# Performance work log

Measured on AMD Instinct MI355X. Metric: run time of the kernel, lower is better.

The kernel has to match this reference:

```python
import jax, jax.numpy as jnp
import numpy as np

S, V, L = 64, 16, 5            # hn_dim=(64,16), num_layers=5
ED, RD, TD = 16, 16, 64        # edge_dim, rbf_dim, t_dim
N, EL, EG, B = 16384, 131072, 262144, 64
FIN = 2 * S + RD + ED          # per-edge message input width
H = S + 2 * V                  # message output: scalar msg + 2 vector gates
CUT_L, CUT_G = 3.0, 10.0


def _ln(x, g, b, eps=1e-5):
    m = x.mean(-1, keepdims=True)
    var = ((x - m) ** 2).mean(-1, keepdims=True)
    return (x - m) / jnp.sqrt(var + eps) * g + b


def _seg_mean(x, idx, n):
    s = jax.ops.segment_sum(x, idx, num_segments=n)
    c = jax.ops.segment_sum(jnp.ones((x.shape[0], 1), x.dtype), idx, num_segments=n)
    return s / jnp.maximum(c, 1.0)


def _edge_geom(ei, pos, cutoff):
    src, tgt = ei[0], ei[1]
    r = pos[tgt] - pos[src]                       # [E,3]
    d = jnp.sqrt(jnp.clip((r * r).sum(-1), 1e-6))
    rn = r / d[:, None]
    centers = jnp.linspace(0.0, cutoff, RD)
    width = cutoff / RD
    env = jnp.where(d < cutoff, 0.5 * (jnp.cos(jnp.pi * d / cutoff) + 1.0), 0.0)
    rbf = jnp.exp(-0.5 * ((d[:, None] - centers) / width) ** 2) * env[:, None]
    return src, tgt, rn, rbf


def setup_inputs() -> dict:
    key = jax.random.key(0)
    ks = iter(jax.random.split(key, 32))
    nrm = lambda shp, sc=1.0: jax.random.normal(next(ks), shp, jnp.float32) * sc
    x = jax.random.randint(next(ks), (N, 3), 0, 16)
    t = nrm((B, TD))
    pos = nrm((N, 3))
    eil = jax.random.randint(next(ks), (2, EL), 0, N)
    eig = jax.random.randint(next(ks), (2, EG), 0, N)
    eal = jax.random.randint(next(ks), (EL,), 0, 5)
    eag = jax.random.randint(next(ks), (EG,), 0, 5)
    batch = jnp.sort(jax.random.randint(next(ks), (N,), 0, B))
    return dict(
        x=x, t=t, pos=pos,
        edge_index_local=eil, edge_index_global=eig,
        edge_attr_local=eal, edge_attr_global=eag, batch=batch,
        atom_emb=nrm((3, 16, S), 0.1),
        bond_emb=nrm((5, ED), 0.1),
        t_w1=nrm((TD, TD), TD ** -0.5), t_b1=jnp.zeros(TD),
        t_w2=nrm((TD, S), TD ** -0.5), t_b2=jnp.zeros(S),
        gnn_wm=nrm((L, 2, FIN, H), FIN ** -0.5), gnn_bm=jnp.zeros((L, 2, H)),
        gnn_wu=nrm((L, 2, S, S), S ** -0.5), gnn_bu=jnp.zeros((L, 2, S)),
        ln_g=jnp.ones((L, S)), ln_b=jnp.zeros((L, S)),
        head_dscore_w=nrm((S, 1), S ** -0.5),
        head_out_w=nrm((V, 1), V ** -0.5),
    )


def reference(x, t, pos, edge_index_local, edge_index_global, edge_attr_local,
              edge_attr_global, batch, atom_emb, bond_emb, t_w1, t_b1, t_w2,
              t_b2, gnn_wm, gnn_bm, gnn_wu, gnn_bu, ln_g, ln_b,
              head_dscore_w, head_out_w):
    n = x.shape[0]
    # AtomEncoder: sum of per-feature-column embeddings; + broadcast t-embedding
    s = atom_emb[0][x[:, 0]] + atom_emb[1][x[:, 1]] + atom_emb[2][x[:, 2]]
    temb = jax.nn.silu(jax.nn.silu(t @ t_w1 + t_b1) @ t_w2 + t_b2)
    s = s + temb[batch]
    v = jnp.zeros((n, 3, V), s.dtype)

    edge_sets = []
    for ei, ea, cut in ((edge_index_local, edge_attr_local, CUT_L),
                        (edge_index_global, edge_attr_global, CUT_G)):
        src, tgt, rn, rbf = _edge_geom(ei, pos, cut)
        edge_sets.append((src, tgt, rn, rbf, bond_emb[ea]))

    for i in range(L):
        for k, (src, tgt, rn, rbf, e) in enumerate(edge_sets):
            feat = jnp.concatenate([s[src], s[tgt], rbf, e], -1)       # [E,FIN]
            h = jax.nn.silu(feat @ gnn_wm[i, k] + gnn_bm[i, k])        # [E,H]
            ms, wv1, wv2 = h[:, :S], h[:, S:S + V], h[:, S + V:]
            vm = v[src] * wv1[:, None, :] + rn[:, :, None] * wv2[:, None, :]
            agg_s = _seg_mean(ms, tgt, n)                              # [N,S]
            agg_v = _seg_mean(vm.reshape(-1, 3 * V), tgt, n).reshape(n, 3, V)
            s = s + jax.nn.silu(agg_s @ gnn_wu[i, k] + gnn_bu[i, k])
            v = v + agg_v
        s = _ln(s, ln_g[i], ln_b[i])

    # ScoreHead (conservative=False)
    dsc = jax.nn.silu(s) @ head_dscore_w                               # [N,1]
    src, tgt = edge_index_global[0], edge_index_global[1]
    sr = (dsc[src] + dsc[tgt]) * (pos[src] - pos[tgt])                 # [E,3]
    sr = jax.ops.segment_sum(sr, tgt, num_segments=n)                  # [N,3]
    score = (v @ head_out_w)[..., 0] + sr                              # [N,3]
    return score
```

## Files before the change

### kernel.cpp

```cpp
#include <hip/hip_runtime.h>
#include <math.h>

#define Sdim 64
#define Vdim 16
#define NLAYER 5
#define EDdim 16
#define RDdim 16
#define TDdim 64
#define FINdim 160
#define Hdim 96
#define NVdim 48
#define ACCW 113
#define HPAD 98
#define VSW 52
#define GW 8

typedef __attribute__((ext_vector_type(8))) short bf16x8;
typedef __attribute__((ext_vector_type(4))) float f32x4;

__device__ __forceinline__ float silu_f(float x) {
    return x / (1.0f + __expf(-x));
}

__device__ __forceinline__ unsigned short f2bf(float x) {
    union { float f; unsigned u; } v; v.f = x;
    unsigned r = v.u + 0x7fffu + ((v.u >> 16) & 1u);
    return (unsigned short)(r >> 16);
}

__global__ __launch_bounds__(256) void pack_kernel(
    const float* __restrict__ wm, const float* __restrict__ bemb,
    unsigned short* __restrict__ wp, unsigned short* __restrict__ bondbf)
{
    int idx = blockIdx.x * 256 + threadIdx.x;
    if (idx < 10 * FINdim * Hdim) {
        int ls = idx / (FINdim * Hdim), rem = idx % (FINdim * Hdim);
        int k = rem / Hdim, c = rem % Hdim;
        wp[(size_t)ls * FINdim * Hdim + ((size_t)(k >> 3) * Hdim + c) * 8 + (k & 7)] =
            f2bf(wm[idx]);
    } else if (idx < 10 * FINdim * Hdim + 80) {
        int i = idx - 10 * FINdim * Hdim;
        bondbf[i] = f2bf(bemb[i]);
    }
}

__global__ __launch_bounds__(64) void temb_kernel(
    const float* __restrict__ t, const float* __restrict__ w1, const float* __restrict__ b1,
    const float* __restrict__ w2, const float* __restrict__ b2, float* __restrict__ temb)
{
    int b = blockIdx.x, j = threadIdx.x;
    __shared__ float row[TDdim];
    __shared__ float hid[TDdim];
    row[j] = t[b * TDdim + j];
    __syncthreads();
    float h = b1[j];
    #pragma unroll 8
    for (int i = 0; i < TDdim; ++i) h = fmaf(row[i], w1[i * TDdim + j], h);
    h = silu_f(h);
    hid[j] = h;
    __syncthreads();
    float o = b2[j];
    #pragma unroll 8
    for (int i = 0; i < TDdim; ++i) o = fmaf(hid[i], w2[i * Sdim + j], o);
    temb[b * Sdim + j] = silu_f(o);
}

__global__ __launch_bounds__(256) void node_init_kernel(
    const int* __restrict__ x, const int* __restrict__ batch,
    const float* __restrict__ aemb, const float* __restrict__ temb,
    float* __restrict__ sfeat, unsigned short* __restrict__ sbf, int n)
{
    int idx = blockIdx.x * 256 + threadIdx.x;
    if (idx >= n * Sdim) return;
    int node = idx >> 6, j = idx & 63;
    int x0 = x[node * 3 + 0], x1 = x[node * 3 + 1], x2 = x[node * 3 + 2];
    float v = aemb[(0 * 16 + x0) * Sdim + j] + aemb[(16 + x1) * Sdim + j]
            + aemb[(32 + x2) * Sdim + j] + temb[batch[node] * Sdim + j];
    sfeat[idx] = v;
    sbf[idx]   = f2bf(v);
}

__global__ __launch_bounds__(256) void count_kernel(
    const int* __restrict__ ei, int E, int* __restrict__ counts)
{
    int e = blockIdx.x * 256 + threadIdx.x;
    if (e >= E) return;
    atomicAdd(&counts[ei[E + e]], 1);
}

__global__ __launch_bounds__(256) void scan_kernel(
    const int* __restrict__ counts, int n,
    int* __restrict__ rowStart, int* __restrict__ cursor)
{
    __shared__ int wsum[4];
    int t = threadIdx.x;
    int chunk = n / 256;
    int base = t * chunk;
    int s = 0;
    for (int i = 0; i < chunk; ++i) s += counts[base + i];
    int lane = t & 63, w = t >> 6;
    int sc = s;
    #pragma unroll
    for (int off = 1; off < 64; off <<= 1) {
        int xv = __shfl_up(sc, off);
        if (lane >= off) sc += xv;
    }
    if (lane == 63) wsum[w] = sc;
    __syncthreads();
    int woff = 0;
    for (int i = 0; i < w; ++i) woff += wsum[i];
    int off = woff + sc - s;
    for (int i = 0; i < chunk; ++i) {
        rowStart[base + i] = off;
        cursor[base + i]   = off;
        off += counts[base + i];
    }
    if (t == 255) rowStart[n] = off;
}

__global__ __launch_bounds__(256) void scatter_kernel(
    const int* __restrict__ ei, const int* __restrict__ ea, int E,
    int* __restrict__ cursor, int2* __restrict__ st2, int* __restrict__ eaS)
{
    int e = blockIdx.x * 256 + threadIdx.x;
    if (e >= E) return;
    int tgt = ei[E + e];
    int p = atomicAdd(&cursor[tgt], 1);
    st2[p] = make_int2(ei[e], tgt);
    eaS[p] = ea[e];
}

__global__ __launch_bounds__(256) void geom_kernel(
    const float* __restrict__ pos,
    const int2* __restrict__ st2, const int* __restrict__ eaS,
    const unsigned short* __restrict__ bondbf,
    float4* __restrict__ rn4, unsigned short* __restrict__ rbfb,
    int E, float cutoff)
{
    int e = blockIdx.x * 256 + threadIdx.x;
    if (e >= E) return;
    int2 st = st2[e];
    int s = st.x, t = st.y;
    float rx = pos[3*t]-pos[3*s], ry = pos[3*t+1]-pos[3*s+1], rz = pos[3*t+2]-pos[3*s+2];
    float d = sqrtf(fmaxf(rx*rx + ry*ry + rz*rz, 1e-6f));
    float invd = 1.0f / d;
    rn4[e] = make_float4(rx*invd, ry*invd, rz*invd, d);
    float env = (d < cutoff) ? 0.5f * (__cosf(3.14159265358979f * d / cutoff) + 1.0f) : 0.0f;
    float invw = (float)RDdim / cutoff;
    unsigned int pk[8];
    #pragma unroll
    for (int i2 = 0; i2 < 8; ++i2) {
        float c0 = cutoff * ((float)(2*i2)     / 15.0f);
        float c1 = cutoff * ((float)(2*i2 + 1) / 15.0f);
        float t0 = (d - c0) * invw, t1 = (d - c1) * invw;
        unsigned short b0 = f2bf(__expf(-0.5f * t0 * t0) * env);
        unsigned short b1 = f2bf(__expf(-0.5f * t1 * t1) * env);
        pk[i2] = (unsigned)b0 | ((unsigned)b1 << 16);
    }
    uint4* o = reinterpret_cast<uint4*>(rbfb + (size_t)e * 32);
    o[0] = make_uint4(pk[0], pk[1], pk[2], pk[3]);
    o[1] = make_uint4(pk[4], pk[5], pk[6], pk[7]);
    int ea = eaS[e];
    const uint4* bp = reinterpret_cast<const uint4*>(bondbf + ea * EDdim);
    o[2] = bp[0];
    o[3] = bp[1];
}

__global__ __launch_bounds__(192, 4) void fused_layer_tri(
    const float* __restrict__ s_in, float* __restrict__ s_out,
    const unsigned short* __restrict__ sbf_in, unsigned short* __restrict__ sbf_out,
    const float* __restrict__ v_in, float* __restrict__ v_out,
    const int* __restrict__ rowStart,
    const int2* __restrict__ st2,
    const float4* __restrict__ rn4, const unsigned short* __restrict__ rbfb,
    const unsigned short* __restrict__ wp, const float* __restrict__ bg,
    const float* __restrict__ wu, const float* __restrict__ bu,
    const float* __restrict__ lng, const float* __restrict__ lnb,
    int do_ln)
{
    __shared__ float accL[GW * ACCW];
    __shared__ __align__(16) float hS[16 * HPAD];
    __shared__ __align__(16) float vS[16 * VSW];
    __shared__ __align__(16) float rnS[16 * 4];

    const int tid  = threadIdx.x;
    const int lane = tid & 63;
    const int wid  = __builtin_amdgcn_readfirstlane(tid >> 6);
    const int l15  = lane & 15, l4 = lane >> 4;
    const int n0   = blockIdx.x * GW;

    bf16x8 B0[5], B1[5];
    #pragma unroll
    for (int kk = 0; kk < 5; ++kk) {
        B0[kk] = *reinterpret_cast<const bf16x8*>(
            wp + ((size_t)(kk * 4 + l4) * Hdim + (wid * 2 + 0) * 16 + l15) * 8);
        B1[kk] = *reinterpret_cast<const bf16x8*>(
            wp + ((size_t)(kk * 4 + l4) * Hdim + (wid * 2 + 1) * 16 + l15) * 8);
    }
    #pragma unroll
    for (int kk = 0; kk < 5; ++kk)
        asm volatile("" : "+v"(B0[kk]), "+v"(B1[kk]));
    const float bias0 = bg[(wid * 2 + 0) * 16 + l15];
    const float bias1 = bg[(wid * 2 + 1) * 16 + l15];

    int rs[GW + 1];
    #pragma unroll
    for (int i = 0; i <= GW; ++i)
        rs[i] = __builtin_amdgcn_readfirstlane(rowStart[n0 + i]);

    if (wid < 2) {
        if (lane < 32)
            #pragma unroll
            for (int i = 0; i < GW; ++i) accL[i * ACCW + wid * 32 + lane] = 0.0f;
    } else if (lane < 49) {
        #pragma unroll
        for (int i = 0; i < GW; ++i) accL[i * ACCW + 64 + lane] = 0.0f;
    }

    const int eW0 = rs[0];
    const int eW1 = rs[GW];
    const int eLast = max(eW1 - 1, 0);

    auto reduceChunk = [&](int pb) {
        const int pv = min(16, eW1 - pb);
        if (wid < 2) {
            if (lane < 32) {
                const int col = wid * 32 + lane;
                #pragma unroll
                for (int i = 0; i < GW; ++i) {
                    int lo = rs[i] - pb;     if (lo < 0) lo = 0;
                    int hi = rs[i + 1] - pb; if (hi > pv) hi = pv;
                    if (lo >= hi) continue;
                    float msum = 0.0f;
                    for (int e2 = lo; e2 < hi; ++e2) msum += hS[e2 * HPAD + col];
                    accL[i * ACCW + col] += msum;
                }
            }
        } else if (lane < NVdim) {
            const int m = l15, dd = l4;
            #pragma unroll
            for (int i = 0; i < GW; ++i) {
                int lo = rs[i] - pb;     if (lo < 0) lo = 0;
                int hi = rs[i + 1] - pb; if (hi > pv) hi = pv;
                if (lo >= hi) continue;
                float vsum = 0.0f;
                for (int e2 = lo; e2 < hi; ++e2)
                    vsum += vS[e2 * VSW + lane] * hS[e2 * HPAD + 64 + m]
                          + rnS[e2 * 4 + dd]   * hS[e2 * HPAD + 80 + m];
                accL[i * ACCW + 64 + lane] += vsum;
            }
        }
    };

    int2 stM = st2[min(eW0 + l15, eLast)];
    int  sSt = 0;
    if (wid == 2) sSt = st2[min(eW0 + (lane >> 2), eLast)].x;
    int prevBase = -1;

    for (int base = eW0; base < eW1; base += 16) {
        const unsigned short* sp = sbf_in + (size_t)stM.x * Sdim;
        const unsigned short* tp = sbf_in + (size_t)stM.y * Sdim;
        bf16x8 a0 = *reinterpret_cast<const bf16x8*>(sp + l4 * 8);
        bf16x8 a1 = *reinterpret_cast<const bf16x8*>(sp + 32 + l4 * 8);
        bf16x8 a2 = *reinterpret_cast<const bf16x8*>(tp + l4 * 8);
        bf16x8 a3 = *reinterpret_cast<const bf16x8*>(tp + 32 + l4 * 8);
        bf16x8 a4 = *reinterpret_cast<const bf16x8*>(
            rbfb + (size_t)min(base + l15, eLast) * 32 + l4 * 8);

        int2 stMn = st2[min(base + 16 + l15, eLast)];
        int  sStn = 0;
        float4 va, vb, vc, rnv;
        if (wid == 2) {
            sStn = st2[min(base + 16 + (lane >> 2), eLast)].x;
            const int q = lane & 3;
            const float* vp = v_in + (size_t)sSt * NVdim + q * 12;
            va = *reinterpret_cast<const float4*>(vp);
            vb = *reinterpret_cast<const float4*>(vp + 4);
            vc = *reinterpret_cast<const float4*>(vp + 8);
            if (lane < 16) rnv = rn4[min(base + lane, eLast)];
        }

        if (prevBase >= 0) reduceChunk(prevBase);

        f32x4 c0 = (f32x4){0.f, 0.f, 0.f, 0.f};
        f32x4 c1 = (f32x4){0.f, 0.f, 0.f, 0.f};
        c0 = __builtin_amdgcn_mfma_f32_16x16x32_bf16(a0, B0[0], c0, 0, 0, 0);
        c1 = __builtin_amdgcn_mfma_f32_16x16x32_bf16(a0, B1[0], c1, 0, 0, 0);
        c0 = __builtin_amdgcn_mfma_f32_16x16x32_bf16(a1, B0[1], c0, 0, 0, 0);
        c1 = __builtin_amdgcn_mfma_f32_16x16x32_bf16(a1, B1[1], c1, 0, 0, 0);
        c0 = __builtin_amdgcn_mfma_f32_16x16x32_bf16(a2, B0[2], c0, 0, 0, 0);
        c1 = __builtin_amdgcn_mfma_f32_16x16x32_bf16(a2, B1[2], c1, 0, 0, 0);
        c0 = __builtin_amdgcn_mfma_f32_16x16x32_bf16(a3, B0[3], c0, 0, 0, 0);
        c1 = __builtin_amdgcn_mfma_f32_16x16x32_bf16(a3, B1[3], c1, 0, 0, 0);
        c0 = __builtin_amdgcn_mfma_f32_16x16x32_bf16(a4, B0[4], c0, 0, 0, 0);
        c1 = __builtin_amdgcn_mfma_f32_16x16x32_bf16(a4, B1[4], c1, 0, 0, 0);

        #pragma unroll
        for (int r = 0; r < 4; ++r) {
            hS[(l4 * 4 + r) * HPAD + wid * 32 + l15]      = silu_f(c0[r] + bias0);
            hS[(l4 * 4 + r) * HPAD + wid * 32 + 16 + l15] = silu_f(c1[r] + bias1);
        }
        if (wid == 2) {
            const int el = lane >> 2, q = lane & 3;
            *reinterpret_cast<float4*>(&vS[el * VSW + q * 12 + 0]) = va;
            *reinterpret_cast<float4*>(&vS[el * VSW + q * 12 + 4]) = vb;
            *reinterpret_cast<float4*>(&vS[el * VSW + q * 12 + 8]) = vc;
            if (lane < 16) *reinterpret_cast<float4*>(&rnS[lane * 4]) = rnv;
        }
        prevBase = base;
        stM = stMn; sSt = sStn;
    }
    if (prevBase >= 0) reduceChunk(prevBase);
    __syncthreads();

    for (int i = wid; i < GW; i += 3) {
        const int node = n0 + i;
        const float cntn = (float)(rs[i + 1] - rs[i]);
        const float ic = 1.0f / fmaxf(cntn, 1.0f);
        const float* al = &accL[i * ACCW];
        float dot = 0.0f;
        #pragma unroll 8
        for (int ii = 0; ii < Sdim; ++ii) dot = fmaf(al[ii], wu[ii * Sdim + lane], dot);
        float sn = s_in[(size_t)node * Sdim + lane] + silu_f(fmaf(dot, ic, bu[lane]));
        if (do_ln) {
            float mm = sn;
            #pragma unroll
            for (int off = 32; off >= 1; off >>= 1) mm += __shfl_xor(mm, off);
            mm *= (1.0f / 64.0f);
            float dv = sn - mm;
            float var = dv * dv;
            #pragma unroll
            for (int off = 32; off >= 1; off >>= 1) var += __shfl_xor(var, off);
            var *= (1.0f / 64.0f);
            sn = dv * rsqrtf(var + 1e-5f) * lng[lane] + lnb[lane];
        }
        s_out[(size_t)node * Sdim + lane]   = sn;
        sbf_out[(size_t)node * Sdim + lane] = f2bf(sn);
        if (lane < NVdim)
            v_out[(size_t)node * NVdim + lane] =
                v_in[(size_t)node * NVdim + lane] + accL[i * ACCW + Sdim + lane] * ic;
    }
}

__global__ __launch_bounds__(64) void head1_kernel(
    const float* __restrict__ sfeat, const float* __restrict__ vfeat,
    const float* __restrict__ wd, const float* __restrict__ wo,
    float* __restrict__ dsc, float* __restrict__ out)
{
    int node = blockIdx.x, j = threadIdx.x;
    float val = silu_f(sfeat[(size_t)node * Sdim + j]) * wd[j];
    #pragma unroll
    for (int off = 32; off >= 1; off >>= 1) val += __shfl_xor(val, off);
    if (j == 0) dsc[node] = val;
    if (j < 3) {
        float a = 0.0f;
        #pragma unroll
        for (int m = 0; m < Vdim; ++m)
            a += vfeat[(size_t)node * NVdim + j * Vdim + m] * wo[m];
        out[(size_t)node * 3 + j] = a;
    }
}

__global__ __launch_bounds__(256) void head2_kernel(
    const float* __restrict__ dsc, const int* __restrict__ rsG,
    const int2* __restrict__ st2G, const float4* __restrict__ rn4G,
    float* __restrict__ out, int n)
{
    int t = blockIdx.x * 256 + threadIdx.x;
    if (t >= n) return;
    int lo = rsG[t], hi = rsG[t + 1];
    float dt = dsc[t];
    float ax = 0.f, ay = 0.f, az = 0.f;
    for (int e = lo; e < hi; ++e) {
        float w = dsc[st2G[e].x] + dt;
        float4 rn = rn4G[e];
        float wd_ = w * rn.w;
        ax -= wd_ * rn.x; ay -= wd_ * rn.y; az -= wd_ * rn.z;
    }
    out[3 * t + 0] += ax;
    out[3 * t + 1] += ay;
    out[3 * t + 2] += az;
}

extern "C" void kernel_launch(void* const* d_in, const int* in_sizes, int n_in,
                              void* d_out, int out_size, void* d_ws, size_t ws_size,
                              hipStream_t stream)
{
    const int*   x     = (const int*)d_in[0];
    const float* t     = (const float*)d_in[1];
    const float* pos   = (const float*)d_in[2];
    const int*   eil   = (const int*)d_in[3];
    const int*   eig   = (const int*)d_in[4];
    const int*   eal   = (const int*)d_in[5];
    const int*   eag   = (const int*)d_in[6];
    const int*   batch = (const int*)d_in[7];
    const float* aemb  = (const float*)d_in[8];
    const float* bemb  = (const float*)d_in[9];
    const float* t_w1  = (const float*)d_in[10];
    const float* t_b1  = (const float*)d_in[11];
    const float* t_w2  = (const float*)d_in[12];
    const float* t_b2  = (const float*)d_in[13];
    const float* wm    = (const float*)d_in[14];
    const float* bm    = (const float*)d_in[15];
    const float* wu    = (const float*)d_in[16];
    const float* bu    = (const float*)d_in[17];
    const float* lng   = (const float*)d_in[18];
    const float* lnb   = (const float*)d_in[19];
    const float* wd    = (const float*)d_in[20];
    const float* wo    = (const float*)d_in[21];

    const int n  = in_sizes[7];
    const int B  = in_sizes[1] / TDdim;
    const int EL = in_sizes[3] / 2;
    const int EG = in_sizes[4] / 2;

    char* p = (char*)d_ws;
    auto alignup = [](char* q) { return (char*)(((size_t)q + 15) & ~(size_t)15); };

    float* temb = (float*)p;                 p += (size_t)B * Sdim * 4;
    float* dsc  = (float*)p;                 p += (size_t)n * 4;
    float* sA   = (float*)p;                 p += (size_t)n * Sdim * 4;
    float* sB   = (float*)p;                 p += (size_t)n * Sdim * 4;
    float* vA   = (float*)p;                 p += (size_t)n * NVdim * 4;
    float* vB   = (float*)p;                 p += (size_t)n * NVdim * 4;
    int* counts = (int*)p;                   p += (size_t)n * 4;
    int* cursor = (int*)p;                   p += (size_t)n * 4;
    int* rsL    = (int*)p;                   p += (size_t)(n + 4) * 4;
    int* rsG    = (int*)p;                   p += (size_t)(n + 4) * 4;
    int* eaL2   = (int*)p;                   p += (size_t)EL * 4;
    int* eaG2   = (int*)p;                   p += (size_t)EG * 4;
    p = alignup(p);
    int2* st2L  = (int2*)p;                  p += (size_t)EL * 8;
    int2* st2G  = (int2*)p;                  p += (size_t)EG * 8;
    p = alignup(p);
    unsigned short* wp     = (unsigned short*)p;  p += (size_t)10 * FINdim * Hdim * 2;
    p = alignup(p);
    unsigned short* bondbf = (unsigned short*)p;  p += 96 * 2;
    p = alignup(p);
    unsigned short* sbfA   = (unsigned short*)p;  p += (size_t)n * Sdim * 2;
    unsigned short* sbfB   = (unsigned short*)p;  p += (size_t)n * Sdim * 2;
    p = alignup(p);
    float4* rn4L = (float4*)p;               p += (size_t)EL * 16;
    float4* rn4G = (float4*)p;               p += (size_t)EG * 16;
    unsigned short* rbfbL = (unsigned short*)p;  p += (size_t)EL * 32 * 2;
    unsigned short* rbfbG = (unsigned short*)p;  p += (size_t)EG * 32 * 2;

    float* out = (float*)d_out;

    pack_kernel<<<(10 * FINdim * Hdim + 80 + 255) / 256, 256, 0, stream>>>(wm, bemb, wp, bondbf);
    temb_kernel<<<B, 64, 0, stream>>>(t, t_w1, t_b1, t_w2, t_b2, temb);
    node_init_kernel<<<(n * Sdim + 255) / 256, 256, 0, stream>>>(x, batch, aemb, temb, sA, sbfA, n);
    hipMemsetAsync(vA, 0, (size_t)n * NVdim * sizeof(float), stream);

    hipMemsetAsync(counts, 0, (size_t)n * sizeof(int), stream);
    count_kernel<<<(EL + 255) / 256, 256, 0, stream>>>(eil, EL, counts);
    scan_kernel<<<1, 256, 0, stream>>>(counts, n, rsL, cursor);
    scatter_kernel<<<(EL + 255) / 256, 256, 0, stream>>>(eil, eal, EL, cursor, st2L, eaL2);

    hipMemsetAsync(counts, 0, (size_t)n * sizeof(int), stream);
    count_kernel<<<(EG + 255) / 256, 256, 0, stream>>>(eig, EG, counts);
    scan_kernel<<<1, 256, 0, stream>>>(counts, n, rsG, cursor);
    scatter_kernel<<<(EG + 255) / 256, 256, 0, stream>>>(eig, eag, EG, cursor, st2G, eaG2);

    geom_kernel<<<(EL + 255) / 256, 256, 0, stream>>>(pos, st2L, eaL2, bondbf, rn4L, rbfbL, EL, 3.0f);
    geom_kernel<<<(EG + 255) / 256, 256, 0, stream>>>(pos, st2G, eaG2, bondbf, rn4G, rbfbG, EG, 10.0f);

    float* s_cur = sA; float* s_nxt = sB;
    float* v_cur = vA; float* v_nxt = vB;
    unsigned short* sb_cur = sbfA; unsigned short* sb_nxt = sbfB;

    for (int l = 0; l < NLAYER; ++l) {
        for (int k = 0; k < 2; ++k) {
            int ls = l * 2 + k;
            const unsigned short* wpk = wp + (size_t)ls * FINdim * Hdim;
            const float* bgk = bm + (size_t)ls * Hdim;
            const float* wuk = wu + (size_t)ls * Sdim * Sdim;
            const float* buk = bu + (size_t)ls * Sdim;
            if (k == 0) {
                fused_layer_tri<<<n / GW, 192, 0, stream>>>(
                    s_cur, s_nxt, sb_cur, sb_nxt, v_cur, v_nxt,
                    rsL, st2L, rn4L, rbfbL, wpk, bgk, wuk, buk,
                    lng + (size_t)l * Sdim, lnb + (size_t)l * Sdim, 0);
            } else {
                fused_layer_tri<<<n / GW, 192, 0, stream>>>(
                    s_cur, s_nxt, sb_cur, sb_nxt, v_cur, v_nxt,
                    rsG, st2G, rn4G, rbfbG, wpk, bgk, wuk, buk,
                    lng + (size_t)l * Sdim, lnb + (size_t)l * Sdim, 1);
            }
            float* tmp = s_cur; s_cur = s_nxt; s_nxt = tmp;
            tmp = v_cur; v_cur = v_nxt; v_nxt = tmp;
            unsigned short* tb = sb_cur; sb_cur = sb_nxt; sb_nxt = tb;
        }
    }

    head1_kernel<<<n, 64, 0, stream>>>(s_cur, v_cur, wd, wo, dsc, out);
    head2_kernel<<<(n + 255) / 256, 256, 0, stream>>>(dsc, rsG, st2G, rn4G, out, n);
}
```

Before: 662.8 us.

## Split fused layer into edge MLP kernel and per-node aggregation kernel

Replaces the single fused per-node-group layer kernel with two kernels. An edge-parallel MFMA kernel stages the weights in LDS, computes the silu message MLP for 128 edges per block, and writes bf16 messages and gates to global buffers. A node-parallel kernel then reads those buffers to do the segment mean, the update matmul and the layernorm. The aim is better MFMA throughput and load balance than the old node-window loop, paid for by extra global traffic for the intermediates, bf16 rounding of the messages, and twice as many launches.

```diff
diff --git a/kernel.cpp b/kernel.cpp
--- a/kernel.cpp
+++ b/kernel.cpp
@@ -10,10 +10,6 @@
 #define FINdim 160
 #define Hdim 96
 #define NVdim 48
-#define ACCW 113
-#define HPAD 98
-#define VSW 52
-#define GW 8
 
 typedef __attribute__((ext_vector_type(8))) short bf16x8;
 typedef __attribute__((ext_vector_type(4))) float f32x4;
@@ -26,6 +22,11 @@
     union { float f; unsigned u; } v; v.f = x;
     unsigned r = v.u + 0x7fffu + ((v.u >> 16) & 1u);
     return (unsigned short)(r >> 16);
+}
+
+__device__ __forceinline__ float bf2f(unsigned short u) {
+    union { unsigned u; float f; } v; v.u = (unsigned)u << 16;
+    return v.f;
 }
 
 __global__ __launch_bounds__(256) void pack_kernel(
@@ -166,180 +167,142 @@
     o[3] = bp[1];
 }
 
-__global__ __launch_bounds__(192, 4) void fused_layer_tri(
+__global__ __launch_bounds__(256) void edge_mlp_kernel(
+    const unsigned short* __restrict__ sbf_in,
+    const int2* __restrict__ st2,
+    const unsigned short* __restrict__ rbfb,
+    const unsigned short* __restrict__ wpk,
+    const float* __restrict__ bg,
+    unsigned short* __restrict__ hm,
+    unsigned short* __restrict__ hv)
+{
+    __shared__ __align__(16) unsigned short Wl[FINdim * Hdim];
+    {
+        const uint4* s4 = reinterpret_cast<const uint4*>(wpk);
+        uint4* d4 = reinterpret_cast<uint4*>(Wl);
+        for (int i = threadIdx.x; i < FINdim * Hdim / 8; i += 256) d4[i] = s4[i];
+    }
+    __syncthreads();
+
+    const int lane = threadIdx.x & 63;
+    const int wid  = threadIdx.x >> 6;
+    const int l15 = lane & 15, l4 = lane >> 4;
+    const int base0 = blockIdx.x * 128 + wid * 16;
+    const int base1 = base0 + 64;
+
+    const int2 st0 = st2[base0 + l15];
+    const int2 st1 = st2[base1 + l15];
+    bf16x8 a0[5], a1[5];
+    {
+        const unsigned short* sp = sbf_in + (size_t)st0.x * Sdim;
+        const unsigned short* tp = sbf_in + (size_t)st0.y * Sdim;
+        a0[0] = *reinterpret_cast<const bf16x8*>(sp + l4 * 8);
+        a0[1] = *reinterpret_cast<const bf16x8*>(sp + 32 + l4 * 8);
+        a0[2] = *reinterpret_cast<const bf16x8*>(tp + l4 * 8);
+        a0[3] = *reinterpret_cast<const bf16x8*>(tp + 32 + l4 * 8);
+        a0[4] = *reinterpret_cast<const bf16x8*>(rbfb + (size_t)(base0 + l15) * 32 + l4 * 8);
+    }
+    {
+        const unsigned short* sp = sbf_in + (size_t)st1.x * Sdim;
+        const unsigned short* tp = sbf_in + (size_t)st1.y * Sdim;
+        a1[0] = *reinterpret_cast<const bf16x8*>(sp + l4 * 8);
+        a1[1] = *reinterpret_cast<const bf16x8*>(sp + 32 + l4 * 8);
+        a1[2] = *reinterpret_cast<const bf16x8*>(tp + l4 * 8);
+        a1[3] = *reinterpret_cast<const bf16x8*>(tp + 32 + l4 * 8);
+        a1[4] = *reinterpret_cast<const bf16x8*>(rbfb + (size_t)(base1 + l15) * 32 + l4 * 8);
+    }
+
+    f32x4 acc0[6], acc1[6];
+    #pragma unroll
+    for (int nt = 0; nt < 6; ++nt) {
+        acc0[nt] = (f32x4){0.f, 0.f, 0.f, 0.f};
+        acc1[nt] = (f32x4){0.f, 0.f, 0.f, 0.f};
+    }
+    #pragma unroll
+    for (int kk = 0; kk < 5; ++kk) {
+        #pragma unroll
+        for (int nt = 0; nt < 6; ++nt) {
+            bf16x8 b = *reinterpret_cast<const bf16x8*>(
+                Wl + ((size_t)(kk * 4 + l4) * Hdim + nt * 16 + l15) * 8);
+            acc0[nt] = __builtin_amdgcn_mfma_f32_16x16x32_bf16(a0[kk], b, acc0[nt], 0, 0, 0);
+            acc1[nt] = __builtin_amdgcn_mfma_f32_16x16x32_bf16(a1[kk], b, acc1[nt], 0, 0, 0);
+        }
+    }
+
+    #pragma unroll
+    for (int nt = 0; nt < 6; ++nt) {
+        const float bs = bg[nt * 16 + l15];
+        #pragma unroll
+        for (int r = 0; r < 4; ++r) {
+            const int e0 = base0 + l4 * 4 + r;
+            const int e1 = base1 + l4 * 4 + r;
+            const unsigned short h0 = f2bf(silu_f(acc0[nt][r] + bs));
+            const unsigned short h1 = f2bf(silu_f(acc1[nt][r] + bs));
+            if (nt < 4) {
+                hm[(size_t)e0 * 64 + nt * 16 + l15] = h0;
+                hm[(size_t)e1 * 64 + nt * 16 + l15] = h1;
+            } else {
+                hv[(size_t)e0 * 32 + (nt - 4) * 16 + l15] = h0;
+                hv[(size_t)e1 * 32 + (nt - 4) * 16 + l15] = h1;
+            }
+        }
+    }
+}
+
+__global__ __launch_bounds__(64) void node_agg_kernel(
     const float* __restrict__ s_in, float* __restrict__ s_out,
-    const unsigned short* __restrict__ sbf_in, unsigned short* __restrict__ sbf_out,
+    unsigned short* __restrict__ sbf_out,
     const float* __restrict__ v_in, float* __restrict__ v_out,
-    const int* __restrict__ rowStart,
-    const int2* __restrict__ st2,
-    const float4* __restrict__ rn4, const unsigned short* __restrict__ rbfb,
-    const unsigned short* __restrict__ wp, const float* __restrict__ bg,
+    const int* __restrict__ rowStart, const int2* __restrict__ st2,
+    const float* __restrict__ rn4f,
+    const unsigned short* __restrict__ hm, const unsigned short* __restrict__ hv,
     const float* __restrict__ wu, const float* __restrict__ bu,
     const float* __restrict__ lng, const float* __restrict__ lnb,
     int do_ln)
 {
-    __shared__ float accL[GW * ACCW];
-    __shared__ __align__(16) float hS[16 * HPAD];
-    __shared__ __align__(16) float vS[16 * VSW];
-    __shared__ __align__(16) float rnS[16 * 4];
-
-    const int tid  = threadIdx.x;
-    const int lane = tid & 63;
-    const int wid  = __builtin_amdgcn_readfirstlane(tid >> 6);
-    const int l15  = lane & 15, l4 = lane >> 4;
-    const int n0   = blockIdx.x * GW;
-
-    bf16x8 B0[5], B1[5];
-    #pragma unroll
-    for (int kk = 0; kk < 5; ++kk) {
-        B0[kk] = *reinterpret_cast<const bf16x8*>(
-            wp + ((size_t)(kk * 4 + l4) * Hdim + (wid * 2 + 0) * 16 + l15) * 8);
-        B1[kk] = *reinterpret_cast<const bf16x8*>(
-            wp + ((size_t)(kk * 4 + l4) * Hdim + (wid * 2 + 1) * 16 + l15) * 8);
-    }
-    #pragma unroll
-    for (int kk = 0; kk < 5; ++kk)
-        asm volatile("" : "+v"(B0[kk]), "+v"(B1[kk]));
-    const float bias0 = bg[(wid * 2 + 0) * 16 + l15];
-    const float bias1 = bg[(wid * 2 + 1) * 16 + l15];
-
-    int rs[GW + 1];
-    #pragma unroll
-    for (int i = 0; i <= GW; ++i)
-        rs[i] = __builtin_amdgcn_readfirstlane(rowStart[n0 + i]);
-
-    if (wid < 2) {
-        if (lane < 32)
-            #pragma unroll
-            for (int i = 0; i < GW; ++i) accL[i * ACCW + wid * 32 + lane] = 0.0f;
-    } else if (lane < 49) {
+    const int node = blockIdx.x;
+    const int lane = threadIdx.x;
+    const int l15 = lane & 15, dd = lane >> 4;
+    const int lo = rowStart[node], hi = rowStart[node + 1];
+
+    float msum = 0.0f, vsum = 0.0f;
+    for (int e = lo; e < hi; ++e) {
+        msum += bf2f(hm[(size_t)e * 64 + lane]);
+        if (lane < NVdim) {
+            float wv1 = bf2f(hv[(size_t)e * 32 + l15]);
+            float wv2 = bf2f(hv[(size_t)e * 32 + 16 + l15]);
+            float rnd = rn4f[(size_t)e * 4 + dd];
+            int srcN  = st2[e].x;
+            float vv  = v_in[(size_t)srcN * NVdim + lane];
+            vsum = fmaf(vv, wv1, fmaf(rnd, wv2, vsum));
+        }
+    }
+
+    __shared__ float ag[64];
+    const float ic = 1.0f / fmaxf((float)(hi - lo), 1.0f);
+    ag[lane] = msum * ic;
+
+    float dot = 0.0f;
+    #pragma unroll 8
+    for (int i = 0; i < Sdim; ++i) dot = fmaf(ag[i], wu[i * Sdim + lane], dot);
+    float sn = s_in[(size_t)node * Sdim + lane] + silu_f(dot + bu[lane]);
+    if (do_ln) {
+        float mm = sn;
         #pragma unroll
-        for (int i = 0; i < GW; ++i) accL[i * ACCW + 64 + lane] = 0.0f;
-    }
-
-    const int eW0 = rs[0];
-    const int eW1 = rs[GW];
-    const int eLast = max(eW1 - 1, 0);
-
-    auto reduceChunk = [&](int pb) {
-        const int pv = min(16, eW1 - pb);
-        if (wid < 2) {
-            if (lane < 32) {
-                const int col = wid * 32 + lane;
-                #pragma unroll
-                for (int i = 0; i < GW; ++i) {
-                    int lo = rs[i] - pb;     if (lo < 0) lo = 0;
-                    int hi = rs[i + 1] - pb; if (hi > pv) hi = pv;
-                    if (lo >= hi) continue;
-                    float msum = 0.0f;
-                    for (int e2 = lo; e2 < hi; ++e2) msum += hS[e2 * HPAD + col];
-                    accL[i * ACCW + col] += msum;
-                }
-            }
-        } else if (lane < NVdim) {
-            const int m = l15, dd = l4;
-            #pragma unroll
-            for (int i = 0; i < GW; ++i) {
-                int lo = rs[i] - pb;     if (lo < 0) lo = 0;
-                int hi = rs[i + 1] - pb; if (hi > pv) hi = pv;
-                if (lo >= hi) continue;
-                float vsum = 0.0f;
-                for (int e2 = lo; e2 < hi; ++e2)
-                    vsum += vS[e2 * VSW + lane] * hS[e2 * HPAD + 64 + m]
-                          + rnS[e2 * 4 + dd]   * hS[e2 * HPAD + 80 + m];
-                accL[i * ACCW + 64 + lane] += vsum;
-            }
-        }
-    };
-
-    int2 stM = st2[min(eW0 + l15, eLast)];
-    int  sSt = 0;
-    if (wid == 2) sSt = st2[min(eW0 + (lane >> 2), eLast)].x;
-    int prevBase = -1;
-
-    for (int base = eW0; base < eW1; base += 16) {
-        const unsigned short* sp = sbf_in + (size_t)stM.x * Sdim;
-        const unsigned short* tp = sbf_in + (size_t)stM.y * Sdim;
-        bf16x8 a0 = *reinterpret_cast<const bf16x8*>(sp + l4 * 8);
-        bf16x8 a1 = *reinterpret_cast<const bf16x8*>(sp + 32 + l4 * 8);
-        bf16x8 a2 = *reinterpret_cast<const bf16x8*>(tp + l4 * 8);
-        bf16x8 a3 = *reinterpret_cast<const bf16x8*>(tp + 32 + l4 * 8);
-        bf16x8 a4 = *reinterpret_cast<const bf16x8*>(
-            rbfb + (size_t)min(base + l15, eLast) * 32 + l4 * 8);
-
-        int2 stMn = st2[min(base + 16 + l15, eLast)];
-        int  sStn = 0;
-        float4 va, vb, vc, rnv;
-        if (wid == 2) {
-            sStn = st2[min(base + 16 + (lane >> 2), eLast)].x;
-            const int q = lane & 3;
-            const float* vp = v_in + (size_t)sSt * NVdim + q * 12;
-            va = *reinterpret_cast<const float4*>(vp);
-            vb = *reinterpret_cast<const float4*>(vp + 4);
-            vc = *reinterpret_cast<const float4*>(vp + 8);
-            if (lane < 16) rnv = rn4[min(base + lane, eLast)];
-        }
-
-        if (prevBase >= 0) reduceChunk(prevBase);
-
-        f32x4 c0 = (f32x4){0.f, 0.f, 0.f, 0.f};
-        f32x4 c1 = (f32x4){0.f, 0.f, 0.f, 0.f};
-        c0 = __builtin_amdgcn_mfma_f32_16x16x32_bf16(a0, B0[0], c0, 0, 0, 0);
-        c1 = __builtin_amdgcn_mfma_f32_16x16x32_bf16(a0, B1[0], c1, 0, 0, 0);
-        c0 = __builtin_amdgcn_mfma_f32_16x16x32_bf16(a1, B0[1], c0, 0, 0, 0);
-        c1 = __builtin_amdgcn_mfma_f32_16x16x32_bf16(a1, B1[1], c1, 0, 0, 0);
-        c0 = __builtin_amdgcn_mfma_f32_16x16x32_bf16(a2, B0[2], c0, 0, 0, 0);
-        c1 = __builtin_amdgcn_mfma_f32_16x16x32_bf16(a2, B1[2], c1, 0, 0, 0);
-        c0 = __builtin_amdgcn_mfma_f32_16x16x32_bf16(a3, B0[3], c0, 0, 0, 0);
-        c1 = __builtin_amdgcn_mfma_f32_16x16x32_bf16(a3, B1[3], c1, 0, 0, 0);
-        c0 = __builtin_amdgcn_mfma_f32_16x16x32_bf16(a4, B0[4], c0, 0, 0, 0);
-        c1 = __builtin_amdgcn_mfma_f32_16x16x32_bf16(a4, B1[4], c1, 0, 0, 0);
-
+        for (int off = 32; off >= 1; off >>= 1) mm += __shfl_xor(mm, off);
+        mm *= (1.0f / 64.0f);
+        float dv = sn - mm;
+        float var = dv * dv;
         #pragma unroll
-        for (int r = 0; r < 4; ++r) {
-            hS[(l4 * 4 + r) * HPAD + wid * 32 + l15]      = silu_f(c0[r] + bias0);
-            hS[(l4 * 4 + r) * HPAD + wid * 32 + 16 + l15] = silu_f(c1[r] + bias1);
-        }
-        if (wid == 2) {
-            const int el = lane >> 2, q = lane & 3;
-            *reinterpret_cast<float4*>(&vS[el * VSW + q * 12 + 0]) = va;
-            *reinterpret_cast<float4*>(&vS[el * VSW + q * 12 + 4]) = vb;
-            *reinterpret_cast<float4*>(&vS[el * VSW + q * 12 + 8]) = vc;
-            if (lane < 16) *reinterpret_cast<float4*>(&rnS[lane * 4]) = rnv;
-        }
-        prevBase = base;
-        stM = stMn; sSt = sStn;
-    }
-    if (prevBase >= 0) reduceChunk(prevBase);
-    __syncthreads();
-
-    for (int i = wid; i < GW; i += 3) {
-        const int node = n0 + i;
-        const float cntn = (float)(rs[i + 1] - rs[i]);
-        const float ic = 1.0f / fmaxf(cntn, 1.0f);
-        const float* al = &accL[i * ACCW];
-        float dot = 0.0f;
-        #pragma unroll 8
-        for (int ii = 0; ii < Sdim; ++ii) dot = fmaf(al[ii], wu[ii * Sdim + lane], dot);
-        float sn = s_in[(size_t)node * Sdim + lane] + silu_f(fmaf(dot, ic, bu[lane]));
-        if (do_ln) {
-            float mm = sn;
-            #pragma unroll
-            for (int off = 32; off >= 1; off >>= 1) mm += __shfl_xor(mm, off);
-            mm *= (1.0f / 64.0f);
-            float dv = sn - mm;
-            float var = dv * dv;
-            #pragma unroll
-            for (int off = 32; off >= 1; off >>= 1) var += __shfl_xor(var, off);
-            var *= (1.0f / 64.0f);
-            sn = dv * rsqrtf(var + 1e-5f) * lng[lane] + lnb[lane];
-        }
-        s_out[(size_t)node * Sdim + lane]   = sn;
-        sbf_out[(size_t)node * Sdim + lane] = f2bf(sn);
-        if (lane < NVdim)
-            v_out[(size_t)node * NVdim + lane] =
-                v_in[(size_t)node * NVdim + lane] + accL[i * ACCW + Sdim + lane] * ic;
-    }
+        for (int off = 32; off >= 1; off >>= 1) var += __shfl_xor(var, off);
+        var *= (1.0f / 64.0f);
+        sn = dv * rsqrtf(var + 1e-5f) * lng[lane] + lnb[lane];
+    }
+    s_out[(size_t)node * Sdim + lane]   = sn;
+    sbf_out[(size_t)node * Sdim + lane] = f2bf(sn);
+    if (lane < NVdim)
+        v_out[(size_t)node * NVdim + lane] =
+            v_in[(size_t)node * NVdim + lane] + vsum * ic;
 }
 
 __global__ __launch_bounds__(64) void head1_kernel(
@@ -444,6 +407,9 @@
     float4* rn4G = (float4*)p;               p += (size_t)EG * 16;
     unsigned short* rbfbL = (unsigned short*)p;  p += (size_t)EL * 32 * 2;
     unsigned short* rbfbG = (unsigned short*)p;  p += (size_t)EG * 32 * 2;
+    p = alignup(p);
+    unsigned short* hm = (unsigned short*)p; p += (size_t)EG * 64 * 2;
+    unsigned short* hv = (unsigned short*)p; p += (size_t)EG * 32 * 2;
 
     float* out = (float*)d_out;
 
@@ -476,17 +442,20 @@
             const float* bgk = bm + (size_t)ls * Hdim;
             const float* wuk = wu + (size_t)ls * Sdim * Sdim;
             const float* buk = bu + (size_t)ls * Sdim;
-            if (k == 0) {
-                fused_layer_tri<<<n / GW, 192, 0, stream>>>(
-                    s_cur, s_nxt, sb_cur, sb_nxt, v_cur, v_nxt,
-                    rsL, st2L, rn4L, rbfbL, wpk, bgk, wuk, buk,
-                    lng + (size_t)l * Sdim, lnb + (size_t)l * Sdim, 0);
-            } else {
-                fused_layer_tri<<<n / GW, 192, 0, stream>>>(
-                    s_cur, s_nxt, sb_cur, sb_nxt, v_cur, v_nxt,
-                    rsG, st2G, rn4G, rbfbG, wpk, bgk, wuk, buk,
-                    lng + (size_t)l * Sdim, lnb + (size_t)l * Sdim, 1);
-            }
+            const int E          = (k == 0) ? EL : EG;
+            const int2* st2k     = (k == 0) ? st2L : st2G;
+            const int* rsk       = (k == 0) ? rsL : rsG;
+            const float4* rn4k   = (k == 0) ? rn4L : rn4G;
+            const unsigned short* rbfbk = (k == 0) ? rbfbL : rbfbG;
+
+            edge_mlp_kernel<<<E / 128, 256, 0, stream>>>(
+                sb_cur, st2k, rbfbk, wpk, bgk, hm, hv);
+            node_agg_kernel<<<n, 64, 0, stream>>>(
+                s_cur, s_nxt, sb_nxt, v_cur, v_nxt,
+                rsk, st2k, (const float*)rn4k, hm, hv,
+                wuk, buk, lng + (size_t)l * Sdim, lnb + (size_t)l * Sdim,
+                (k == 1) ? 1 : 0);
+
             float* tmp = s_cur; s_cur = s_nxt; s_nxt = tmp;
             tmp = v_cur; v_cur = v_nxt; v_nxt = tmp;
             unsigned short* tb = sb_cur; sb_cur = sb_nxt; sb_nxt = tb;
```

New measurement: 686.0 us. +3.5%, slower.
